# Performance work log

Measured on AMD Instinct MI355X. Metric: run time of the kernel, lower is better.

The kernel has to match this reference:

```python
import jax, jax.numpy as jnp
import numpy as np
import math

D_MODEL = 1024
N_HEADS = 16
Q_PROJ = D_MODEL // 4
KV_PROJ = D_MODEL // 4
DH = D_MODEL // N_HEADS
LN_EPS = 1e-5


def _layernorm(x, gamma, beta):
    mu = jnp.mean(x, axis=-1, keepdims=True)
    var = jnp.mean(jnp.square(x - mu), axis=-1, keepdims=True)
    return (x - mu) * jax.lax.rsqrt(var + LN_EPS) * gamma + beta


def setup_inputs() -> dict:
    key = jax.random.key(0)
    ks = jax.random.split(key, 7)
    B, S = 2, 2048
    x = jax.random.normal(ks[0], (B, S, D_MODEL), dtype=jnp.float32)
    W_dq = 0.01 * jax.random.normal(ks[1], (D_MODEL, Q_PROJ), dtype=jnp.float32)
    W_uq = 0.01 * jax.random.normal(ks[2], (Q_PROJ, D_MODEL), dtype=jnp.float32)
    W_dkv = 0.01 * jax.random.normal(ks[3], (D_MODEL, KV_PROJ), dtype=jnp.float32)
    W_ukv = 0.01 * jax.random.normal(ks[4], (KV_PROJ, 2 * D_MODEL), dtype=jnp.float32)
    W_o = 0.01 * jax.random.normal(ks[5], (D_MODEL, D_MODEL), dtype=jnp.float32)
    return {
        "x": x,
        "W_dq": W_dq, "W_uq": W_uq,
        "q_ln_g": jnp.ones((Q_PROJ,), jnp.float32), "q_ln_b": jnp.zeros((Q_PROJ,), jnp.float32),
        "W_dkv": W_dkv, "W_ukv": W_ukv,
        "kv_ln_g": jnp.ones((KV_PROJ,), jnp.float32), "kv_ln_b": jnp.zeros((KV_PROJ,), jnp.float32),
        "W_o": W_o,
    }


def reference(x, W_dq, W_uq, q_ln_g, q_ln_b, W_dkv, W_ukv, kv_ln_g, kv_ln_b, W_o):
    B, S, D = x.shape
    # low-rank Q path
    cq = _layernorm(x @ W_dq, q_ln_g, q_ln_b)          # [B,S,q_proj]
    Q = cq @ W_uq                                       # [B,S,D]
    # low-rank KV path
    ckv = _layernorm(x @ W_dkv, kv_ln_g, kv_ln_b)       # [B,S,kv_proj]
    KV = ckv @ W_ukv                                    # [B,S,2D]
    K, V = KV[..., :D], KV[..., D:]
    q = Q.reshape(B, S, N_HEADS, DH)
    k = K.reshape(B, S, N_HEADS, DH)
    v = V.reshape(B, S, N_HEADS, DH)
    scores = jnp.einsum("bqhd,bkhd->bhqk", q, k) / math.sqrt(float(DH))
    # faithful to original: multiply by tril mask, then set exact zeros to -inf
    mask = jnp.tril(jnp.ones((S, S), dtype=scores.dtype))
    scores = scores * mask
    scores = jnp.where(scores == 0, -jnp.inf, scores)
    attn = jax.nn.softmax(scores, axis=-1)
    out = jnp.einsum("bhqk,bkhd->bqhd", attn, v).reshape(B, S, D)
    return out @ W_o.T
```

## Files before the change

kernel.cpp:

```cpp
#include <hip/hip_runtime.h>

typedef __bf16 bf16;
typedef __bf16 bf16x4 __attribute__((ext_vector_type(4)));
typedef __bf16 bf16x8 __attribute__((ext_vector_type(8)));
typedef float f32x4 __attribute__((ext_vector_type(4)));

#define D_MODEL 1024
#define PROJ    256
#define SEQ     2048
#define BATCH   2
#define TOK     4096
#define NH      16
#define DH      64
#define NEG_BIG (-1e30f)
#define QSCALE  0.18033688011112042f

#if __has_builtin(__builtin_amdgcn_exp2f)
#define EXP2(x) __builtin_amdgcn_exp2f(x)
#else
#define EXP2(x) exp2f(x)
#endif

typedef __attribute__((address_space(3))) unsigned int  lds_u32;
typedef __attribute__((address_space(1))) unsigned int  glb_u32;

__device__ __forceinline__ void gl2lds16(const void* gsrc, void* ldst) {
    __builtin_amdgcn_global_load_lds((const glb_u32*)gsrc, (lds_u32*)ldst, 16, 0, 0);
}

#define VM_WAIT(N) asm volatile("s_waitcnt vmcnt(" #N ")" ::: "memory")
#define SCHEDB()   __builtin_amdgcn_sched_barrier(0)
#define SBAR()     __builtin_amdgcn_s_barrier()

template <int CTRL>
__device__ __forceinline__ float dppmov(float x) {
    int i = __builtin_bit_cast(int, x);
    i = __builtin_amdgcn_update_dpp(i, i, CTRL, 0xf, 0xf, false);
    return __builtin_bit_cast(float, i);
}
__device__ __forceinline__ float rowsum16(float v) {
    v += dppmov<0xB1>(v);
    v += dppmov<0x4E>(v);
    v += dppmov<0x141>(v);
    v += dppmov<0x140>(v);
    return v;
}

__global__ __launch_bounds__(256) void prep_kernel(
    const float* __restrict__ W_o, const float* __restrict__ x,
    const float* __restrict__ W_dq, const float* __restrict__ W_dkv,
    const float* __restrict__ W_uq, const float* __restrict__ W_ukv,
    bf16* __restrict__ Wo16, bf16* __restrict__ x16,
    bf16* __restrict__ Wt_dq, bf16* __restrict__ Wt_dkv,
    bf16* __restrict__ Wt_uq, bf16* __restrict__ Wt_ukv) {
    if (blockIdx.x < 320) {
        __shared__ float tile[64][65];
        int t = blockIdx.x;
        const float* src; bf16* dst; int R, C;
        if (t < 64)       { src = W_dq;  dst = Wt_dq;  R = 1024; C = 256; }
        else if (t < 128) { src = W_dkv; dst = Wt_dkv; R = 1024; C = 256;  t -= 64; }
        else if (t < 192) { src = W_uq;  dst = Wt_uq;  R = 256;  C = 1024; t -= 128; }
        else              { src = W_ukv; dst = Wt_ukv; R = 256;  C = 2048; t -= 192; }
        const int tilesC = C >> 6;
        const int r0 = (t / tilesC) << 6;
        const int c0 = (t % tilesC) << 6;
        const int tr = threadIdx.x >> 6;
        const int tc = threadIdx.x & 63;
#pragma unroll
        for (int i = 0; i < 16; ++i)
            tile[tr * 16 + i][tc] = src[(size_t)(r0 + tr * 16 + i) * C + c0 + tc];
        __syncthreads();
#pragma unroll
        for (int i = 0; i < 16; ++i)
            dst[(size_t)(c0 + tr * 16 + i) * R + r0 + tc] =
                (bf16)tile[tc][tr * 16 + i];
    } else {
        const int NW = 262144;
        const int NX = 1048576;
        for (int i = (blockIdx.x - 320) * 256 + threadIdx.x; i < NW + NX;
             i += 1024 * 256) {
            if (i < NW) {
                float4 v = ((const float4*)W_o)[i];
                bf16x4 p;
                p[0] = (bf16)v.x; p[1] = (bf16)v.y;
                p[2] = (bf16)v.z; p[3] = (bf16)v.w;
                ((bf16x4*)Wo16)[i] = p;
            } else {
                int j = i - NW;
                float4 v = ((const float4*)x)[j];
                bf16x4 p;
                p[0] = (bf16)v.x; p[1] = (bf16)v.y;
                p[2] = (bf16)v.z; p[3] = (bf16)v.w;
                ((bf16x4*)x16)[j] = p;
            }
        }
    }
}

__global__ __launch_bounds__(256) void gemm_ln_kernel(
    const bf16* __restrict__ x16,
    const bf16* __restrict__ Wt_q, const bf16* __restrict__ Wt_kv,
    const float* __restrict__ q_g, const float* __restrict__ q_b,
    const float* __restrict__ kv_g, const float* __restrict__ kv_b,
    bf16* __restrict__ cq, bf16* __restrict__ ckv) {
    __shared__ alignas(16) bf16 xA[3][16 * 32];
    __shared__ alignas(16) bf16 wB[3][256 * 32];
    __shared__ float red1[4][16];
    __shared__ float red2[4][16];

    const int K = 1024;
    const bf16* Wt = blockIdx.y ? Wt_kv : Wt_q;
    const float* gamma = blockIdx.y ? kv_g : q_g;
    const float* beta  = blockIdx.y ? kv_b : q_b;
    bf16* out = blockIdx.y ? ckv : cq;

    const int m0 = blockIdx.x * 16;
    const int wv = threadIdx.x >> 6;
    const int lane = threadIdx.x & 63;
    const int g = lane >> 4;
    const int ln16 = lane & 15;

    const int crow = lane >> 2;
    const int ckc = lane & 3;
    const bf16* gx = x16 + (size_t)(m0 + crow) * K + ckc * 8;
    const bf16* gw = Wt + (size_t)(64 * wv + crow) * K + ckc * 8;

    f32x4 acc[4] = {};
    const int nst = K >> 5;

#pragma unroll
    for (int s = 0; s < 2; ++s) {
        gl2lds16(gx + s * 32, (char*)xA + s * 1024);
#pragma unroll
        for (int i = 0; i < 4; ++i)
            gl2lds16(gw + (size_t)i * 16 * K + s * 32,
                     (char*)wB + s * 16384 + wv * 4096 + i * 1024);
    }
    VM_WAIT(0); SCHEDB(); SBAR();

    for (int s = 0; s < nst; ++s) {
        if (s > 0) {
            if (s + 1 < nst) { VM_WAIT(5); } else { VM_WAIT(0); }
            SCHEDB(); SBAR();
        }
        if (s + 2 < nst) {
            const int b3 = (s + 2) % 3;
            const int k2 = (s + 2) * 32;
            gl2lds16(gx + k2, (char*)xA + b3 * 1024);
#pragma unroll
            for (int i = 0; i < 4; ++i)
                gl2lds16(gw + (size_t)i * 16 * K + k2,
                         (char*)wB + b3 * 16384 + wv * 4096 + i * 1024);
        }
        const bf16* cx = &xA[s % 3][0];
        const bf16* cw = &wB[s % 3][0];
        bf16x8 a = *(const bf16x8*)(cx + ln16 * 32 + g * 8);
        bf16x8 bb[4];
#pragma unroll
        for (int t = 0; t < 4; ++t)
            bb[t] = *(const bf16x8*)(cw + (wv * 64 + 16 * t + ln16) * 32 + g * 8);
        __builtin_amdgcn_s_setprio(1);
#pragma unroll
        for (int t = 0; t < 4; ++t)
            acc[t] = __builtin_amdgcn_mfma_f32_16x16x32_bf16(a, bb[t], acc[t], 0, 0, 0);
        __builtin_amdgcn_s_setprio(0);
    }

    float s1[4], s2[4];
#pragma unroll
    for (int r = 0; r < 4; ++r) {
        float a = 0.f, b = 0.f;
#pragma unroll
        for (int t = 0; t < 4; ++t) { float v = acc[t][r]; a += v; b += v * v; }
        s1[r] = rowsum16(a); s2[r] = rowsum16(b);
    }
    if (ln16 == 0) {
#pragma unroll
        for (int r = 0; r < 4; ++r) {
            red1[wv][g * 4 + r] = s1[r];
            red2[wv][g * 4 + r] = s2[r];
        }
    }
    __syncthreads();
#pragma unroll
    for (int r = 0; r < 4; ++r) {
        int rl = g * 4 + r;
        float t1 = red1[0][rl] + red1[1][rl] + red1[2][rl] + red1[3][rl];
        float t2 = red2[0][rl] + red2[1][rl] + red2[2][rl] + red2[3][rl];
        float mu = t1 * (1.0f / 256.0f);
        float var = t2 * (1.0f / 256.0f) - mu * mu;
        float rs = rsqrtf(var + 1e-5f);
        int row = m0 + rl;
#pragma unroll
        for (int t = 0; t < 4; ++t) {
            int col = wv * 64 + 16 * t + ln16;
            float v = (acc[t][r] - mu) * rs * gamma[col] + beta[col];
            out[(size_t)row * PROJ + col] = (bf16)v;
        }
    }
}

__device__ __forceinline__ void gemm_body128(
    const bf16* __restrict__ A, const bf16* __restrict__ Bt,
    bf16* __restrict__ C, bf16* __restrict__ C2, int K,
    int bx, int by, int mode, bf16* tA, bf16* tB) {
    const int w = threadIdx.x >> 6;
    const int lane = threadIdx.x & 63;
    const int g = lane >> 4;
    const int ln16 = lane & 15;
    const int wr = w >> 1;
    const int wc = w & 1;

    const int m0 = bx * 128;
    const int n0 = by * 128;

    const int crow = lane >> 2;
    const int ckc = lane & 3;
    const bf16* gA0 = A  + (size_t)(m0 + 32 * w + crow) * K + ckc * 8;
    const bf16* gA1 = gA0 + (size_t)16 * K;
    const bf16* gB0 = Bt + (size_t)(n0 + 32 * w + crow) * K + ckc * 8;
    const bf16* gB1 = gB0 + (size_t)16 * K;

    f32x4 acc[4][4] = {};
    const int nst = K >> 5;

#pragma unroll
    for (int s = 0; s < 2; ++s) {
        gl2lds16(gA0 + s * 32, (char*)tA + s * 8192 + w * 2048);
        gl2lds16(gA1 + s * 32, (char*)tA + s * 8192 + w * 2048 + 1024);
        gl2lds16(gB0 + s * 32, (char*)tB + s * 8192 + w * 2048);
        gl2lds16(gB1 + s * 32, (char*)tB + s * 8192 + w * 2048 + 1024);
    }
    VM_WAIT(0); SCHEDB(); SBAR();

    for (int s = 0; s < nst; ++s) {
        if (s > 0) {
            if (s + 1 < nst) { VM_WAIT(4); } else { VM_WAIT(0); }
            SCHEDB(); SBAR();
        }
        if (s + 2 < nst) {
            const int b3 = (s + 2) % 3;
            const int k2 = (s + 2) * 32;
            gl2lds16(gA0 + k2, (char*)tA + b3 * 8192 + w * 2048);
            gl2lds16(gA1 + k2, (char*)tA + b3 * 8192 + w * 2048 + 1024);
            gl2lds16(gB0 + k2, (char*)tB + b3 * 8192 + w * 2048);
            gl2lds16(gB1 + k2, (char*)tB + b3 * 8192 + w * 2048 + 1024);
        }
        const bf16* cA = tA + (s % 3) * 4096;
        const bf16* cB = tB + (s % 3) * 4096;

        bf16x8 af[4], bfr[4];
#pragma unroll
        for (int q = 0; q < 4; ++q)
            af[q] = *(const bf16x8*)(cA + (wr * 64 + q * 16 + ln16) * 32 + g * 8);
#pragma unroll
        for (int t = 0; t < 4; ++t)
            bfr[t] = *(const bf16x8*)(cB + (wc * 64 + t * 16 + ln16) * 32 + g * 8);
        __builtin_amdgcn_s_setprio(1);
#pragma unroll
        for (int q = 0; q < 4; ++q)
#pragma unroll
            for (int t = 0; t < 4; ++t)
                acc[q][t] = __builtin_amdgcn_mfma_f32_16x16x32_bf16(
                    af[q], bfr[t], acc[q][t], 0, 0, 0);
        __builtin_amdgcn_s_setprio(0);
    }

#pragma unroll
    for (int q = 0; q < 4; ++q)
#pragma unroll
        for (int t = 0; t < 4; ++t) {
            const int col = n0 + wc * 64 + t * 16 + ln16;
            const int tok0 = m0 + wr * 64 + q * 16 + g * 4;
            if (mode == 2 && col >= 1024) {
                int cc = col - 1024;
                int h = cc >> 6, d = cc & 63;
                int b = tok0 >> 11, sq = tok0 & 2047;
                bf16x4 pk;
#pragma unroll
                for (int r = 0; r < 4; ++r) pk[r] = (bf16)acc[q][t][r];
                *(bf16x4*)(C2 + ((size_t)((b * 16 + h) * 64 + d) * SEQ + sq)) = pk;
            } else {
#pragma unroll
                for (int r = 0; r < 4; ++r) {
                    int row = tok0 + r;
                    float v = acc[q][t][r];
                    if (mode == 1) v *= QSCALE;
                    int h = col >> 6, d = col & 63;
                    int b = row >> 11, sq = row & 2047;
                    C[((size_t)((b * 16 + h) * 2048 + sq)) * 64 + d] = (bf16)v;
                }
            }
        }
}

__global__ __launch_bounds__(256) void gemm_qkv_kernel(
    const bf16* __restrict__ cq, const bf16* __restrict__ Wt_uq,
    const bf16* __restrict__ ckv, const bf16* __restrict__ Wt_ukv,
    bf16* __restrict__ Qh, bf16* __restrict__ Kh, bf16* __restrict__ Vt) {
    __shared__ alignas(16) bf16 tA[3][128 * 32];
    __shared__ alignas(16) bf16 tB[3][128 * 32];
    const int i = blockIdx.x;
    if (i < 256) {
        gemm_body128(cq, Wt_uq, Qh, nullptr, PROJ,
                     i >> 3, i & 7, 1, &tA[0][0], &tB[0][0]);
    } else {
        const int j = i - 256;
        gemm_body128(ckv, Wt_ukv, Kh, Vt, PROJ,
                     j >> 4, j & 15, 2, &tA[0][0], &tB[0][0]);
    }
}

__device__ __forceinline__ void gemm_body(
    const bf16* __restrict__ A, const bf16* __restrict__ Bt,
    float* __restrict__ C, int N, int K,
    int bx, int by, bf16* tA, bf16* tB) {
    const int w = threadIdx.x >> 6;
    const int lane = threadIdx.x & 63;
    const int g = lane >> 4;
    const int ln16 = lane & 15;
    const int wr = w >> 1;
    const int wc = w & 1;

    const int m0 = bx * 64;
    const int n0 = by * 128;

    const int crow = lane >> 2;
    const int ckc = lane & 3;
    const bf16* gA  = A  + (size_t)(m0 + w * 16 + crow) * K + ckc * 8;
    const bf16* gB0 = Bt + (size_t)(n0 + w * 16 + crow) * K + ckc * 8;
    const bf16* gB1 = Bt + (size_t)(n0 + 64 + w * 16 + crow) * K + ckc * 8;

    f32x4 acc[2][4] = {};
    const int nst = K >> 5;

#pragma unroll
    for (int s = 0; s < 2; ++s) {
        gl2lds16(gA + s * 32, (char*)tA + s * 4096 + w * 1024);
        gl2lds16(gB0 + s * 32, (char*)tB + s * 8192 + w * 1024);
        gl2lds16(gB1 + s * 32, (char*)tB + s * 8192 + 4096 + w * 1024);
    }
    VM_WAIT(0); SCHEDB(); SBAR();

    for (int s = 0; s < nst; ++s) {
        if (s > 0) {
            if (s + 1 < nst) { VM_WAIT(3); } else { VM_WAIT(0); }
            SCHEDB(); SBAR();
        }
        if (s + 2 < nst) {
            const int b3 = (s + 2) % 3;
            const int k2 = (s + 2) * 32;
            gl2lds16(gA + k2, (char*)tA + b3 * 4096 + w * 1024);
            gl2lds16(gB0 + k2, (char*)tB + b3 * 8192 + w * 1024);
            gl2lds16(gB1 + k2, (char*)tB + b3 * 8192 + 4096 + w * 1024);
        }
        const bf16* cA = tA + (s % 3) * 2048;
        const bf16* cB = tB + (s % 3) * 4096;

        bf16x8 af[2], bfr[4];
#pragma unroll
        for (int q = 0; q < 2; ++q)
            af[q] = *(const bf16x8*)(cA + (wr * 32 + q * 16 + ln16) * 32 + g * 8);
#pragma unroll
        for (int t = 0; t < 4; ++t)
            bfr[t] = *(const bf16x8*)(cB + (wc * 64 + t * 16 + ln16) * 32 + g * 8);
        __builtin_amdgcn_s_setprio(1);
#pragma unroll
        for (int q = 0; q < 2; ++q)
#pragma unroll
            for (int t = 0; t < 4; ++t)
                acc[q][t] = __builtin_amdgcn_mfma_f32_16x16x32_bf16(
                    af[q], bfr[t], acc[q][t], 0, 0, 0);
        __builtin_amdgcn_s_setprio(0);
    }

#pragma unroll
    for (int q = 0; q < 2; ++q)
#pragma unroll
        for (int t = 0; t < 4; ++t) {
            const int col = n0 + wc * 64 + t * 16 + ln16;
            const int tok0 = m0 + wr * 32 + q * 16 + g * 4;
#pragma unroll
            for (int r = 0; r < 4; ++r)
                C[(size_t)(tok0 + r) * N + col] = acc[q][t][r];
        }
}

__global__ __launch_bounds__(256) void gemm_o_kernel(
    const bf16* __restrict__ A, const bf16* __restrict__ Bt,
    float* __restrict__ C, int M, int N, int K) {
    __shared__ alignas(16) bf16 tA[3][64 * 32];
    __shared__ alignas(16) bf16 tB[3][128 * 32];
    gemm_body(A, Bt, C, N, K, blockIdx.x, blockIdx.y, &tA[0][0], &tB[0][0]);
}

__device__ __forceinline__ void qk_exp_pack(
    int k0, int q, bool masked, int g, int ln16,
    bf16x8 aq0, bf16x8 aq1, const bf16x8* Kf,
    bf16x8& P1, bf16x8& P2) {
    f32x4 sc[4];
    __builtin_amdgcn_s_setprio(1);
#pragma unroll
    for (int c = 0; c < 4; ++c) {
        f32x4 z = {};
        z = __builtin_amdgcn_mfma_f32_16x16x32_bf16(Kf[2 * c], aq0, z, 0, 0, 0);
        z = __builtin_amdgcn_mfma_f32_16x16x32_bf16(Kf[2 * c + 1], aq1, z, 0, 0, 0);
        sc[c] = z;
    }
    __builtin_amdgcn_s_setprio(0);
    if (masked) {
        const int kb = k0 + 8 * g;
#pragma unroll
        for (int c = 0; c < 4; ++c)
#pragma unroll
            for (int r = 0; r < 4; ++r) {
                int kcol = kb + (c & 1) * 4 + r + ((c >> 1) << 5);
                if (kcol > q) sc[c][r] = NEG_BIG;
            }
    }
#pragma unroll
    for (int c = 0; c < 4; ++c)
#pragma unroll
        for (int r = 0; r < 4; ++r) sc[c][r] = EXP2(sc[c][r]);
#pragma unroll
    for (int r = 0; r < 4; ++r) {
        P1[r] = (bf16)sc[0][r]; P1[4 + r] = (bf16)sc[1][r];
        P2[r] = (bf16)sc[2][r]; P2[4 + r] = (bf16)sc[3][r];
    }
}

__device__ __forceinline__ void pv_accum(
    bf16x8 P1, bf16x8 P2, const bf16x8* Vf, bf16x8 vones,
    f32x4* o, f32x4& oli) {
    __builtin_amdgcn_s_setprio(1);
#pragma unroll
    for (int t = 0; t < 4; ++t) {
        o[t] = __builtin_amdgcn_mfma_f32_16x16x32_bf16(Vf[2 * t], P1, o[t], 0, 0, 0);
        o[t] = __builtin_amdgcn_mfma_f32_16x16x32_bf16(Vf[2 * t + 1], P2, o[t], 0, 0, 0);
    }
    oli = __builtin_amdgcn_mfma_f32_16x16x32_bf16(vones, P1, oli, 0, 0, 0);
    oli = __builtin_amdgcn_mfma_f32_16x16x32_bf16(vones, P2, oli, 0, 0, 0);
    __builtin_amdgcn_s_setprio(0);
}

__global__ __launch_bounds__(128) void attn_kernel(
    const bf16* __restrict__ Qh, const bf16* __restrict__ Kh,
    const bf16* __restrict__ Vt, bf16* __restrict__ AT) {
    __shared__ alignas(128) bf16 kbuf[2][64 * 64];

    const int lane = threadIdx.x & 63;
    const int g = lane >> 4;
    const int ln16 = lane & 15;
    const int wv = threadIdx.x >> 6;

    const int bh = blockIdx.x & 31;
    const int qsuper = 31 - (blockIdx.x >> 5);
    const int nt = qsuper + 1;
    const int qb = qsuper * 64 + wv * 32;

    const bf16* Kbh = Kh + (size_t)bh * SEQ * DH;
    const bf16* Vbh = Vt + (size_t)bh * DH * SEQ;

    const int rho = lane >> 3;
    const int sl  = lane & 7;
    int kofs[4];
#pragma unroll
    for (int i = 0; i < 4; ++i) {
        const int row = 32 * wv + 8 * i + rho;
        const int c = sl ^ ((rho & 3) | ((i & 1) << 2));
        kofs[i] = row * 64 + c * 8;
    }

    const int row_base = ((ln16 & 12) << 1) + (ln16 & 3);
    int kro[4];
#pragma unroll
    for (int c = 0; c < 4; ++c) {
        const int row = row_base + (c & 1) * 4 + ((c >> 1) << 5);
        const int fr = (row & 3) | (((row >> 3) & 1) << 2);
        kro[c] = row * 128 + (g ^ fr) * 16;
    }

    const bf16* vp[4];
#pragma unroll
    for (int t = 0; t < 4; ++t)
        vp[t] = Vbh + (size_t)(16 * t + ln16) * SEQ + 8 * g;

    bf16x8 aq[2][2];
#pragma unroll
    for (int hh = 0; hh < 2; ++hh) {
        const bf16* qp = Qh + ((size_t)bh * SEQ + qb + 16 * hh + ln16) * DH + g * 8;
        aq[hh][0] = *(const bf16x8*)qp;
        aq[hh][1] = *(const bf16x8*)(qp + 32);
    }

    bf16x8 vones;
#pragma unroll
    for (int i = 0; i < 8; ++i) vones[i] = (bf16)1.0f;

    f32x4 o0[4] = {}, o1[4] = {};
    f32x4 oli0 = {}, oli1 = {};

    {
        const int t1 = (nt > 1) ? 1 : 0;
#pragma unroll
        for (int i = 0; i < 4; ++i) {
            gl2lds16(Kbh + kofs[i], (char*)kbuf + wv * 4096 + i * 1024);
            gl2lds16(Kbh + (size_t)t1 * 64 * 64 + kofs[i],
                     (char*)kbuf + 8192 + wv * 4096 + i * 1024);
        }
    }
    VM_WAIT(0); SCHEDB(); SBAR();

    for (int kt = 0; kt < nt; ++kt) {
        if (kt > 0) { SBAR(); }
        const char* kb = (const char*)kbuf + (kt & 1) * 8192;
        bf16x8 Kf[8];
#pragma unroll
        for (int c = 0; c < 4; ++c) {
            Kf[2 * c]     = *(const bf16x8*)(kb + kro[c]);
            Kf[2 * c + 1] = *(const bf16x8*)(kb + (kro[c] ^ 64));
        }
        asm volatile("s_waitcnt lgkmcnt(0)" ::: "memory");
        SCHEDB(); SBAR();

        const int k0 = kt * 64;
        bf16x8 Vf[8];
        SCHEDB();
#pragma unroll
        for (int t = 0; t < 4; ++t) {
            Vf[2 * t]     = *(const bf16x8*)(vp[t] + k0);
            Vf[2 * t + 1] = *(const bf16x8*)(vp[t] + k0 + 32);
        }
        SCHEDB();
        {
            const int kt2 = (kt + 2 < nt) ? kt + 2 : nt - 1;
            char* kd = (char*)kbuf + (kt & 1) * 8192 + wv * 4096;
#pragma unroll
            for (int i = 0; i < 4; ++i)
                gl2lds16(Kbh + (size_t)kt2 * 64 * 64 + kofs[i], kd + i * 1024);
        }
        SCHEDB();

        const bool msk = (kt == qsuper);
        bf16x8 P1a, P2a, P1b, P2b;
        qk_exp_pack(k0, qb + ln16, msk, g, ln16,
                    aq[0][0], aq[0][1], Kf, P1a, P2a);
        qk_exp_pack(k0, qb + 16 + ln16, msk, g, ln16,
                    aq[1][0], aq[1][1], Kf, P1b, P2b);

        VM_WAIT(4); SCHEDB();
        pv_accum(P1a, P2a, Vf, vones, o0, oli0);
        pv_accum(P1b, P2b, Vf, vones, o1, oli1);
    }
    VM_WAIT(0);

    const float inv0 = 1.0f / oli0[0];
    const float inv1 = 1.0f / oli1[0];
    const int b = bh >> 4, h = bh & 15;
    const size_t tok0 = (size_t)(b * SEQ + qb + ln16) * D_MODEL + h * DH;
    const size_t tok1 = (size_t)(b * SEQ + qb + 16 + ln16) * D_MODEL + h * DH;
#pragma unroll
    for (int t = 0; t < 4; ++t) {
        bf16x4 pk0, pk1;
#pragma unroll
        for (int r = 0; r < 4; ++r) {
            pk0[r] = (bf16)(o0[t][r] * inv0);
            pk1[r] = (bf16)(o1[t][r] * inv1);
        }
        *(bf16x4*)(AT + tok0 + 16 * t + 4 * g) = pk0;
        *(bf16x4*)(AT + tok1 + 16 * t + 4 * g) = pk1;
    }
}

extern "C" void kernel_launch(void* const* d_in, const int* in_sizes, int n_in,
                              void* d_out, int out_size, void* d_ws, size_t ws_size,
                              hipStream_t stream) {
    const float* x     = (const float*)d_in[0];
    const float* W_dq  = (const float*)d_in[1];
    const float* W_uq  = (const float*)d_in[2];
    const float* q_g   = (const float*)d_in[3];
    const float* q_b   = (const float*)d_in[4];
    const float* W_dkv = (const float*)d_in[5];
    const float* W_ukv = (const float*)d_in[6];
    const float* kv_g  = (const float*)d_in[7];
    const float* kv_b  = (const float*)d_in[8];
    const float* W_o   = (const float*)d_in[9];

    char* ws = (char*)d_ws;
    size_t off = 0;
    bf16* Wo16   = (bf16*)(ws + off); off += (size_t)D_MODEL * D_MODEL * 2;
    bf16* Wt_dq  = (bf16*)(ws + off); off += (size_t)PROJ * D_MODEL * 2;
    bf16* Wt_dkv = (bf16*)(ws + off); off += (size_t)PROJ * D_MODEL * 2;
    bf16* Wt_uq  = (bf16*)(ws + off); off += (size_t)D_MODEL * PROJ * 2;
    bf16* Wt_ukv = (bf16*)(ws + off); off += (size_t)(2 * D_MODEL) * PROJ * 2;
    bf16* x16    = (bf16*)(ws + off); off += (size_t)TOK * D_MODEL * 2;
    bf16* cq     = (bf16*)(ws + off); off += (size_t)TOK * PROJ * 2;
    bf16* ckv    = (bf16*)(ws + off); off += (size_t)TOK * PROJ * 2;
    bf16* Qh     = (bf16*)(ws + off); off += (size_t)TOK * D_MODEL * 2;
    bf16* Kh     = (bf16*)(ws + off); off += (size_t)TOK * D_MODEL * 2;
    bf16* Vt     = (bf16*)(ws + off); off += (size_t)TOK * D_MODEL * 2;
    bf16* AT     = (bf16*)(ws + off); off += (size_t)TOK * D_MODEL * 2;

    prep_kernel<<<1344, 256, 0, stream>>>(
        W_o, x, W_dq, W_dkv, W_uq, W_ukv,
        Wo16, x16, Wt_dq, Wt_dkv, Wt_uq, Wt_ukv);

    gemm_ln_kernel<<<dim3(TOK / 16, 2), 256, 0, stream>>>(
        x16, Wt_dq, Wt_dkv, q_g, q_b, kv_g, kv_b, cq, ckv);

    gemm_qkv_kernel<<<768, 256, 0, stream>>>(cq, Wt_uq, ckv, Wt_ukv, Qh, Kh, Vt);

    attn_kernel<<<1024, 128, 0, stream>>>(Qh, Kh, Vt, AT);

    gemm_o_kernel<<<dim3(TOK / 64, D_MODEL / 128), 256, 0, stream>>>(
        AT, Wo16, (float*)d_out, TOK, D_MODEL, D_MODEL);
}
```

Measured before the change: 202.3 us.

## Stage V through LDS in attention and enlarge gemm_ln row tile

The attention kernel now uses four waves of 16 query rows each, down from two waves of 32, and stages V tiles into double-buffered swizzled LDS with async global-to-LDS loads. Before, each wave read V straight from global memory on every tile. The goal is to share K/V loads across more waves and raise occupancy with more, smaller waves. The gemm_ln kernel moves to 32-row tiles with 512 threads, so each W tile loaded into LDS is reused over twice as many rows. Costs include more LDS per attention block, a different wait/barrier structure, and fewer attention blocks' worth of per-wave work.

```diff
diff --git a/kernel.cpp b/kernel.cpp
--- a/kernel.cpp
+++ b/kernel.cpp
@@ -29,6 +29,7 @@
 }
 
 #define VM_WAIT(N) asm volatile("s_waitcnt vmcnt(" #N ")" ::: "memory")
+#define LGKM0      asm volatile("s_waitcnt lgkmcnt(0)" ::: "memory")
 #define SCHEDB()   __builtin_amdgcn_sched_barrier(0)
 #define SBAR()     __builtin_amdgcn_s_barrier()
 
@@ -97,16 +98,16 @@
     }
 }
 
-__global__ __launch_bounds__(256) void gemm_ln_kernel(
+__global__ __launch_bounds__(512) void gemm_ln_kernel(
     const bf16* __restrict__ x16,
     const bf16* __restrict__ Wt_q, const bf16* __restrict__ Wt_kv,
     const float* __restrict__ q_g, const float* __restrict__ q_b,
     const float* __restrict__ kv_g, const float* __restrict__ kv_b,
     bf16* __restrict__ cq, bf16* __restrict__ ckv) {
-    __shared__ alignas(16) bf16 xA[3][16 * 32];
+    __shared__ alignas(16) bf16 xA[3][32 * 32];
     __shared__ alignas(16) bf16 wB[3][256 * 32];
-    __shared__ float red1[4][16];
-    __shared__ float red2[4][16];
+    __shared__ float red1[8][16];
+    __shared__ float red2[8][16];
 
     const int K = 1024;
     const bf16* Wt = blockIdx.y ? Wt_kv : Wt_q;
@@ -114,51 +115,53 @@
     const float* beta  = blockIdx.y ? kv_b : q_b;
     bf16* out = blockIdx.y ? ckv : cq;
 
-    const int m0 = blockIdx.x * 16;
+    const int m0 = blockIdx.x * 32;
     const int wv = threadIdx.x >> 6;
     const int lane = threadIdx.x & 63;
     const int g = lane >> 4;
     const int ln16 = lane & 15;
+    const int wr = wv >> 2;
+    const int wc = wv & 3;
 
     const int crow = lane >> 2;
     const int ckc = lane & 3;
-    const bf16* gx = x16 + (size_t)(m0 + crow) * K + ckc * 8;
-    const bf16* gw = Wt + (size_t)(64 * wv + crow) * K + ckc * 8;
+    const bf16* gx0 = x16 + (size_t)(m0 + crow) * K + ckc * 8;
+    const bf16* gx1 = x16 + (size_t)(m0 + 16 + crow) * K + ckc * 8;
+    const bf16* gw0 = Wt + (size_t)(32 * wv + crow) * K + ckc * 8;
+    const bf16* gw1 = Wt + (size_t)(32 * wv + 16 + crow) * K + ckc * 8;
 
     f32x4 acc[4] = {};
     const int nst = K >> 5;
 
 #pragma unroll
     for (int s = 0; s < 2; ++s) {
-        gl2lds16(gx + s * 32, (char*)xA + s * 1024);
-#pragma unroll
-        for (int i = 0; i < 4; ++i)
-            gl2lds16(gw + (size_t)i * 16 * K + s * 32,
-                     (char*)wB + s * 16384 + wv * 4096 + i * 1024);
+        gl2lds16(gx0 + s * 32, (char*)xA + s * 2048);
+        gl2lds16(gx1 + s * 32, (char*)xA + s * 2048 + 1024);
+        gl2lds16(gw0 + s * 32, (char*)wB + s * 16384 + wv * 2048);
+        gl2lds16(gw1 + s * 32, (char*)wB + s * 16384 + wv * 2048 + 1024);
     }
     VM_WAIT(0); SCHEDB(); SBAR();
 
     for (int s = 0; s < nst; ++s) {
         if (s > 0) {
-            if (s + 1 < nst) { VM_WAIT(5); } else { VM_WAIT(0); }
+            if (s + 1 < nst) { VM_WAIT(4); } else { VM_WAIT(0); }
             SCHEDB(); SBAR();
         }
         if (s + 2 < nst) {
             const int b3 = (s + 2) % 3;
             const int k2 = (s + 2) * 32;
-            gl2lds16(gx + k2, (char*)xA + b3 * 1024);
-#pragma unroll
-            for (int i = 0; i < 4; ++i)
-                gl2lds16(gw + (size_t)i * 16 * K + k2,
-                         (char*)wB + b3 * 16384 + wv * 4096 + i * 1024);
+            gl2lds16(gx0 + k2, (char*)xA + b3 * 2048);
+            gl2lds16(gx1 + k2, (char*)xA + b3 * 2048 + 1024);
+            gl2lds16(gw0 + k2, (char*)wB + b3 * 16384 + wv * 2048);
+            gl2lds16(gw1 + k2, (char*)wB + b3 * 16384 + wv * 2048 + 1024);
         }
         const bf16* cx = &xA[s % 3][0];
         const bf16* cw = &wB[s % 3][0];
-        bf16x8 a = *(const bf16x8*)(cx + ln16 * 32 + g * 8);
+        bf16x8 a = *(const bf16x8*)(cx + (wr * 16 + ln16) * 32 + g * 8);
         bf16x8 bb[4];
 #pragma unroll
         for (int t = 0; t < 4; ++t)
-            bb[t] = *(const bf16x8*)(cw + (wv * 64 + 16 * t + ln16) * 32 + g * 8);
+            bb[t] = *(const bf16x8*)(cw + (wc * 64 + 16 * t + ln16) * 32 + g * 8);
         __builtin_amdgcn_s_setprio(1);
 #pragma unroll
         for (int t = 0; t < 4; ++t)
@@ -185,15 +188,17 @@
 #pragma unroll
     for (int r = 0; r < 4; ++r) {
         int rl = g * 4 + r;
-        float t1 = red1[0][rl] + red1[1][rl] + red1[2][rl] + red1[3][rl];
-        float t2 = red2[0][rl] + red2[1][rl] + red2[2][rl] + red2[3][rl];
+        float t1 = red1[wr * 4 + 0][rl] + red1[wr * 4 + 1][rl] +
+                   red1[wr * 4 + 2][rl] + red1[wr * 4 + 3][rl];
+        float t2 = red2[wr * 4 + 0][rl] + red2[wr * 4 + 1][rl] +
+                   red2[wr * 4 + 2][rl] + red2[wr * 4 + 3][rl];
         float mu = t1 * (1.0f / 256.0f);
         float var = t2 * (1.0f / 256.0f) - mu * mu;
         float rs = rsqrtf(var + 1e-5f);
-        int row = m0 + rl;
+        int row = m0 + wr * 16 + rl;
 #pragma unroll
         for (int t = 0; t < 4; ++t) {
-            int col = wv * 64 + 16 * t + ln16;
+            int col = wc * 64 + 16 * t + ln16;
             float v = (acc[t][r] - mu) * rs * gamma[col] + beta[col];
             out[(size_t)row * PROJ + col] = (bf16)v;
         }
@@ -443,10 +448,11 @@
     __builtin_amdgcn_s_setprio(0);
 }
 
-__global__ __launch_bounds__(128) void attn_kernel(
+__global__ __launch_bounds__(256) void attn_kernel(
     const bf16* __restrict__ Qh, const bf16* __restrict__ Kh,
     const bf16* __restrict__ Vt, bf16* __restrict__ AT) {
     __shared__ alignas(128) bf16 kbuf[2][64 * 64];
+    __shared__ alignas(128) bf16 vbuf[2][64 * 64];
 
     const int lane = threadIdx.x & 63;
     const int g = lane >> 4;
@@ -456,119 +462,110 @@
     const int bh = blockIdx.x & 31;
     const int qsuper = 31 - (blockIdx.x >> 5);
     const int nt = qsuper + 1;
-    const int qb = qsuper * 64 + wv * 32;
+    const int qb = qsuper * 64 + wv * 16;
+    const int q = qb + ln16;
 
     const bf16* Kbh = Kh + (size_t)bh * SEQ * DH;
     const bf16* Vbh = Vt + (size_t)bh * DH * SEQ;
 
     const int rho = lane >> 3;
     const int sl  = lane & 7;
-    int kofs[4];
-#pragma unroll
-    for (int i = 0; i < 4; ++i) {
-        const int row = 32 * wv + 8 * i + rho;
+    int kofs[2];
+    size_t vofs[2];
+#pragma unroll
+    for (int i = 0; i < 2; ++i) {
+        const int row = 16 * wv + 8 * i + rho;
         const int c = sl ^ ((rho & 3) | ((i & 1) << 2));
         kofs[i] = row * 64 + c * 8;
+        vofs[i] = (size_t)row * SEQ + c * 8;
     }
 
     const int row_base = ((ln16 & 12) << 1) + (ln16 & 3);
-    int kro[4];
+    int kro[4], vro[4];
 #pragma unroll
     for (int c = 0; c < 4; ++c) {
         const int row = row_base + (c & 1) * 4 + ((c >> 1) << 5);
         const int fr = (row & 3) | (((row >> 3) & 1) << 2);
         kro[c] = row * 128 + (g ^ fr) * 16;
     }
-
-    const bf16* vp[4];
-#pragma unroll
-    for (int t = 0; t < 4; ++t)
-        vp[t] = Vbh + (size_t)(16 * t + ln16) * SEQ + 8 * g;
-
-    bf16x8 aq[2][2];
-#pragma unroll
-    for (int hh = 0; hh < 2; ++hh) {
-        const bf16* qp = Qh + ((size_t)bh * SEQ + qb + 16 * hh + ln16) * DH + g * 8;
-        aq[hh][0] = *(const bf16x8*)qp;
-        aq[hh][1] = *(const bf16x8*)(qp + 32);
-    }
+#pragma unroll
+    for (int t = 0; t < 4; ++t) {
+        const int d = 16 * t + ln16;
+        const int fd = (d & 3) | (((d >> 3) & 1) << 2);
+        vro[t] = d * 128 + (g ^ fd) * 16;
+    }
+
+    const bf16* qp = Qh + ((size_t)bh * SEQ + q) * DH + g * 8;
+    bf16x8 aq0 = *(const bf16x8*)qp, aq1 = *(const bf16x8*)(qp + 32);
 
     bf16x8 vones;
 #pragma unroll
     for (int i = 0; i < 8; ++i) vones[i] = (bf16)1.0f;
 
-    f32x4 o0[4] = {}, o1[4] = {};
-    f32x4 oli0 = {}, oli1 = {};
+    f32x4 o[4] = {};
+    f32x4 oli = {};
 
     {
         const int t1 = (nt > 1) ? 1 : 0;
 #pragma unroll
-        for (int i = 0; i < 4; ++i) {
-            gl2lds16(Kbh + kofs[i], (char*)kbuf + wv * 4096 + i * 1024);
+        for (int i = 0; i < 2; ++i) {
+            gl2lds16(Kbh + kofs[i], (char*)kbuf + wv * 2048 + i * 1024);
+            gl2lds16(Vbh + vofs[i], (char*)vbuf + wv * 2048 + i * 1024);
+        }
+#pragma unroll
+        for (int i = 0; i < 2; ++i) {
             gl2lds16(Kbh + (size_t)t1 * 64 * 64 + kofs[i],
-                     (char*)kbuf + 8192 + wv * 4096 + i * 1024);
+                     (char*)kbuf + 8192 + wv * 2048 + i * 1024);
+            gl2lds16(Vbh + vofs[i] + (size_t)t1 * 64,
+                     (char*)vbuf + 8192 + wv * 2048 + i * 1024);
         }
     }
     VM_WAIT(0); SCHEDB(); SBAR();
 
     for (int kt = 0; kt < nt; ++kt) {
-        if (kt > 0) { SBAR(); }
+        if (kt > 0) {
+            if (kt + 1 < nt) { VM_WAIT(4); } else { VM_WAIT(0); }
+            SCHEDB(); SBAR();
+        }
         const char* kb = (const char*)kbuf + (kt & 1) * 8192;
-        bf16x8 Kf[8];
+        const char* vb = (const char*)vbuf + (kt & 1) * 8192;
+        bf16x8 Kf[8], Vf[8];
 #pragma unroll
         for (int c = 0; c < 4; ++c) {
             Kf[2 * c]     = *(const bf16x8*)(kb + kro[c]);
             Kf[2 * c + 1] = *(const bf16x8*)(kb + (kro[c] ^ 64));
         }
-        asm volatile("s_waitcnt lgkmcnt(0)" ::: "memory");
-        SCHEDB(); SBAR();
-
-        const int k0 = kt * 64;
-        bf16x8 Vf[8];
-        SCHEDB();
 #pragma unroll
         for (int t = 0; t < 4; ++t) {
-            Vf[2 * t]     = *(const bf16x8*)(vp[t] + k0);
-            Vf[2 * t + 1] = *(const bf16x8*)(vp[t] + k0 + 32);
-        }
-        SCHEDB();
-        {
-            const int kt2 = (kt + 2 < nt) ? kt + 2 : nt - 1;
-            char* kd = (char*)kbuf + (kt & 1) * 8192 + wv * 4096;
-#pragma unroll
-            for (int i = 0; i < 4; ++i)
-                gl2lds16(Kbh + (size_t)kt2 * 64 * 64 + kofs[i], kd + i * 1024);
-        }
-        SCHEDB();
-
-        const bool msk = (kt == qsuper);
-        bf16x8 P1a, P2a, P1b, P2b;
-        qk_exp_pack(k0, qb + ln16, msk, g, ln16,
-                    aq[0][0], aq[0][1], Kf, P1a, P2a);
-        qk_exp_pack(k0, qb + 16 + ln16, msk, g, ln16,
-                    aq[1][0], aq[1][1], Kf, P1b, P2b);
-
-        VM_WAIT(4); SCHEDB();
-        pv_accum(P1a, P2a, Vf, vones, o0, oli0);
-        pv_accum(P1b, P2b, Vf, vones, o1, oli1);
-    }
-    VM_WAIT(0);
-
-    const float inv0 = 1.0f / oli0[0];
-    const float inv1 = 1.0f / oli1[0];
+            Vf[2 * t]     = *(const bf16x8*)(vb + vro[t]);
+            Vf[2 * t + 1] = *(const bf16x8*)(vb + (vro[t] ^ 64));
+        }
+        LGKM0; SCHEDB(); SBAR();
+        if (kt + 2 < nt) {
+            const size_t k0n = (size_t)(kt + 2) * 64;
+            char* kd = (char*)kbuf + (kt & 1) * 8192 + wv * 2048;
+            char* vd = (char*)vbuf + (kt & 1) * 8192 + wv * 2048;
+#pragma unroll
+            for (int i = 0; i < 2; ++i) {
+                gl2lds16(Kbh + k0n * 64 + kofs[i], kd + i * 1024);
+                gl2lds16(Vbh + vofs[i] + k0n, vd + i * 1024);
+            }
+        }
+
+        bf16x8 P1, P2;
+        qk_exp_pack(kt * 64, q, kt == qsuper, g, ln16, aq0, aq1, Kf, P1, P2);
+        pv_accum(P1, P2, Vf, vones, o, oli);
+    }
+
+    const float inv = 1.0f / oli[0];
     const int b = bh >> 4, h = bh & 15;
-    const size_t tok0 = (size_t)(b * SEQ + qb + ln16) * D_MODEL + h * DH;
-    const size_t tok1 = (size_t)(b * SEQ + qb + 16 + ln16) * D_MODEL + h * DH;
+    const size_t tok = (size_t)(b * SEQ + q) * D_MODEL + h * DH;
 #pragma unroll
     for (int t = 0; t < 4; ++t) {
-        bf16x4 pk0, pk1;
-#pragma unroll
-        for (int r = 0; r < 4; ++r) {
-            pk0[r] = (bf16)(o0[t][r] * inv0);
-            pk1[r] = (bf16)(o1[t][r] * inv1);
-        }
-        *(bf16x4*)(AT + tok0 + 16 * t + 4 * g) = pk0;
-        *(bf16x4*)(AT + tok1 + 16 * t + 4 * g) = pk1;
+        bf16x4 pk;
+#pragma unroll
+        for (int r = 0; r < 4; ++r) pk[r] = (bf16)(o[t][r] * inv);
+        *(bf16x4*)(AT + tok + 16 * t + 4 * g) = pk;
     }
 }
 
@@ -605,12 +602,12 @@
         W_o, x, W_dq, W_dkv, W_uq, W_ukv,
         Wo16, x16, Wt_dq, Wt_dkv, Wt_uq, Wt_ukv);
 
-    gemm_ln_kernel<<<dim3(TOK / 16, 2), 256, 0, stream>>>(
+    gemm_ln_kernel<<<dim3(TOK / 32, 2), 512, 0, stream>>>(
         x16, Wt_dq, Wt_dkv, q_g, q_b, kv_g, kv_b, cq, ckv);
 
     gemm_qkv_kernel<<<768, 256, 0, stream>>>(cq, Wt_uq, ckv, Wt_ukv, Qh, Kh, Vt);
 
-    attn_kernel<<<1024, 128, 0, stream>>>(Qh, Kh, Vt, AT);
+    attn_kernel<<<1024, 256, 0, stream>>>(Qh, Kh, Vt, AT);
 
     gemm_o_kernel<<<dim3(TOK / 64, D_MODEL / 128), 256, 0, stream>>>(
         AT, Wo16, (float*)d_out, TOK, D_MODEL, D_MODEL);
```

Measured after the change: 174.1 us (median of 2 runs). -14.0%, faster.
